# Kernel optimization log

Measured on AMD Instinct MI355X. Metric: run time of the kernel, lower is better.

The kernel has to match this reference:

```python
import jax, jax.numpy as jnp
import numpy as np

B, NA, DIN, H, DOUT = 8192, 32, 8, 64, 8  # B must be divisible by NA (final reshape)


def setup_inputs() -> dict:
    key = jax.random.key(0)
    ks = jax.random.split(key, 9)
    rn = lambda k, shp, s=1.0: jax.random.normal(k, shp, dtype=jnp.float32) * s
    return {
        "x": rn(ks[0], (B, NA, DIN)),
        "laplacian": jax.random.uniform(ks[1], (B, NA, 1), dtype=jnp.float32),
        "W_in": rn(ks[2], (H, DIN), 1.0 / np.sqrt(DIN)),
        "b_in": rn(ks[3], (H,), 0.01),
        "Aq": rn(ks[4], (H, H)),   # torch.randn init in original
        "Ak": rn(ks[5], (H, H)),
        "Av": rn(ks[6], (H, H)),
        "W_out": rn(ks[7], (DOUT, H), 1.0 / np.sqrt(H)),
        "b_out": rn(ks[8], (DOUT,), 0.01),
    }


def reference(x, laplacian, W_in, b_in, Aq, Ak, Av, W_out, b_out):
    silu = jax.nn.silu
    # mlp_in = SiLU(Linear); kron(laplacian, ones(1,1,H)) == broadcast of (B,na,1) mask
    h = silu(x @ W_in.T + b_in) * laplacian            # (B, na, H)
    # Q/K/V: weight @ h^T with swish; attention is over the HIDDEN axis (H x H scores)
    Q = silu(jnp.einsum('ij,bnj->bin', Aq, h))         # (B, H, na)
    K = silu(jnp.einsum('ij,bnj->bni', Ak, h))         # (B, na, H)
    V = silu(jnp.einsum('ij,bnj->bin', Av, h))         # (B, H, na)
    A = jax.nn.softmax(jnp.einsum('bin,bnj->bij', Q, K), axis=2)  # (B, H, H), softmax dim=2
    attn = silu(jnp.einsum('bij,bjn->bni', A, V))      # (B, na, H)
    # mlp_out = SiLU(Linear), masked again, mean over nodes, reshape (B/na, na, O)
    y = silu(attn @ W_out.T + b_out) * laplacian       # (B, na, O)
    return y.mean(axis=1).reshape(-1, NA, DOUT)        # (B/NA, NA, O)
```

## Files before the change

kernel.cpp:

```cpp
#include <hip/hip_runtime.h>

#define NB   8192
#define NA   32
#define DIN  8
#define HID  64
#define DOUT 8

typedef float     v4f __attribute__((ext_vector_type(4)));
typedef _Float16  v4h __attribute__((ext_vector_type(4)));

__device__ __forceinline__ float silu_f(float x) {
    return __fdividef(x, 1.0f + __expf(-x));
}

__device__ __forceinline__ v4h cvt4(v4f a) {
    v4h r;
    r[0] = (_Float16)a[0]; r[1] = (_Float16)a[1];
    r[2] = (_Float16)a[2]; r[3] = (_Float16)a[3];
    return r;
}

__device__ __forceinline__ v4h silu_cvt4(v4f a) {
    v4f s;
    s[0] = silu_f(a[0]); s[1] = silu_f(a[1]);
    s[2] = silu_f(a[2]); s[3] = silu_f(a[3]);
    return cvt4(s);
}

#define MFMA16(A, B, C) __builtin_amdgcn_mfma_f32_16x16x16f16((A), (B), (C), 0, 0, 0)

__global__ __launch_bounds__(512, 4) void attn_mfma_kernel(
    const float* __restrict__ x,
    const float* __restrict__ lap,
    const float* __restrict__ W_in,
    const float* __restrict__ b_in,
    const float* __restrict__ Aq,
    const float* __restrict__ Ak,
    const float* __restrict__ Av,
    const float* __restrict__ W_out,
    const float* __restrict__ b_out,
    float* __restrict__ out)
{
    __shared__ _Float16 wlds[3][16][64][4];
    __shared__ _Float16 hlds[8][4][64][4];

    const int t  = threadIdx.x;
    const int l  = t & 63;
    const int w  = t >> 6;
    const int lm = l & 15;
    const int lg = l >> 4;

    {
        const float* mats[3] = {Aq, Ak, Av};
        #pragma unroll
        for (int m = 0; m < 3; ++m) {
            #pragma unroll
            for (int f = 0; f < 2; ++f) {
                const int fid = w * 2 + f;
                const int it = fid >> 2, ks = fid & 3;
                v4f v = *(const v4f*)(mats[m] + (lm + 16 * it) * 64 + 16 * ks + 4 * lg);
                *(v4h*)&wlds[m][fid][l][0] = cvt4(v);
            }
        }
    }

    v4h zh = {};
    v4f zf = {};
    v4h winf[4];
    #pragma unroll
    for (int jt = 0; jt < 4; ++jt)
        winf[jt] = (lg < 2) ? cvt4(*(const v4f*)(W_in + (lm + 16 * jt) * 8 + 4 * lg)) : zh;
    v4h woutf[4];
    #pragma unroll
    for (int ks = 0; ks < 4; ++ks)
        woutf[ks] = (lm < 8) ? cvt4(*(const v4f*)(W_out + lm * 64 + 16 * ks + 4 * lg)) : zh;
    float binf[4];
    #pragma unroll
    for (int jt = 0; jt < 4; ++jt) binf[jt] = b_in[lm + 16 * jt];
    const float boutf = (lm < 8) ? b_out[lm] : 0.0f;

    __syncthreads();

    const int b = blockIdx.x * 8 + w;

    v4f lapv[2];
    lapv[0] = *(const v4f*)(lap + b * 32 + 4 * lg);
    lapv[1] = *(const v4f*)(lap + b * 32 + 16 + 4 * lg);

    v4h xf[2];
    #pragma unroll
    for (int nt = 0; nt < 2; ++nt)
        xf[nt] = (lg < 2) ? cvt4(*(const v4f*)(x + b * 256 + (lm + 16 * nt) * 8 + 4 * lg)) : zh;

    const int pr = l ^ lg;
    v4h hf[2][4];
    #pragma unroll
    for (int nt = 0; nt < 2; ++nt) {
        #pragma unroll
        for (int jt = 0; jt < 4; ++jt) {
            v4f hc = MFMA16(xf[nt], winf[jt], zf);
            #pragma unroll
            for (int r = 0; r < 4; ++r) {
                float hv = silu_f(hc[r] + binf[jt]) * lapv[nt][r];
                const int lr   = (4 * lg + r) | ((lm >> 2) << 4);
                const int phys = lr ^ (lm >> 2);
                hlds[w][jt][phys][lm & 3] = (_Float16)hv;
            }
        }
        __builtin_amdgcn_s_waitcnt(0);
        #pragma unroll
        for (int ks = 0; ks < 4; ++ks)
            hf[nt][ks] = *(v4h*)&hlds[w][ks][pr][0];
        __builtin_amdgcn_s_waitcnt(0);
    }

    v4h qf[2][4];
    {
        v4f acc[2][4] = {};
        #pragma unroll
        for (int it = 0; it < 4; ++it)
            #pragma unroll
            for (int ks = 0; ks < 4; ++ks) {
                v4h bw = *(v4h*)&wlds[0][it * 4 + ks][l][0];
                #pragma unroll
                for (int nt = 0; nt < 2; ++nt)
                    acc[nt][it] = MFMA16(hf[nt][ks], bw, acc[nt][it]);
            }
        #pragma unroll
        for (int nt = 0; nt < 2; ++nt)
            #pragma unroll
            for (int it = 0; it < 4; ++it) qf[nt][it] = silu_cvt4(acc[nt][it]);
    }
    v4h kf[2][4];
    {
        v4f acc[2][4] = {};
        #pragma unroll
        for (int it = 0; it < 4; ++it)
            #pragma unroll
            for (int ks = 0; ks < 4; ++ks) {
                v4h bw = *(v4h*)&wlds[1][it * 4 + ks][l][0];
                #pragma unroll
                for (int nt = 0; nt < 2; ++nt)
                    acc[nt][it] = MFMA16(hf[nt][ks], bw, acc[nt][it]);
            }
        #pragma unroll
        for (int nt = 0; nt < 2; ++nt)
            #pragma unroll
            for (int it = 0; it < 4; ++it) kf[nt][it] = silu_cvt4(acc[nt][it]);
    }
    v4h vf[4][2];
    {
        v4f acc[4][2] = {};
        #pragma unroll
        for (int it = 0; it < 4; ++it)
            #pragma unroll
            for (int ks = 0; ks < 4; ++ks) {
                v4h aw = *(v4h*)&wlds[2][it * 4 + ks][l][0];
                #pragma unroll
                for (int nt = 0; nt < 2; ++nt)
                    acc[it][nt] = MFMA16(aw, hf[nt][ks], acc[it][nt]);
            }
        #pragma unroll
        for (int it = 0; it < 4; ++it)
            #pragma unroll
            for (int nt = 0; nt < 2; ++nt) vf[it][nt] = silu_cvt4(acc[it][nt]);
    }

    v4f ya[2] = {};
    #pragma unroll
    for (int it = 0; it < 4; ++it) {
        v4f s[4] = {};
        #pragma unroll
        for (int jt = 0; jt < 4; ++jt)
            #pragma unroll
            for (int ns = 0; ns < 2; ++ns)
                s[jt] = MFMA16(kf[ns][jt], qf[ns][it], s[jt]);

        float mx = s[0][0];
        #pragma unroll
        for (int jt = 0; jt < 4; ++jt)
            #pragma unroll
            for (int r = 0; r < 4; ++r) mx = fmaxf(mx, s[jt][r]);
        mx = fmaxf(mx, __shfl_xor(mx, 16, 64));
        mx = fmaxf(mx, __shfl_xor(mx, 32, 64));
        float sum = 0.0f;
        #pragma unroll
        for (int jt = 0; jt < 4; ++jt)
            #pragma unroll
            for (int r = 0; r < 4; ++r) {
                float e = __expf(s[jt][r] - mx);
                s[jt][r] = e;
                sum += e;
            }
        sum += __shfl_xor(sum, 16, 64);
        sum += __shfl_xor(sum, 32, 64);
        const float inv = __fdividef(1.0f, sum);
        v4h pf[4];
        #pragma unroll
        for (int jt = 0; jt < 4; ++jt) pf[jt] = cvt4(s[jt] * inv);

        v4f pv[2] = {};
        #pragma unroll
        for (int js = 0; js < 4; ++js)
            #pragma unroll
            for (int nt = 0; nt < 2; ++nt)
                pv[nt] = MFMA16(pf[js], vf[js][nt], pv[nt]);

        #pragma unroll
        for (int nt = 0; nt < 2; ++nt)
            ya[nt] = MFMA16(silu_cvt4(pv[nt]), woutf[it], ya[nt]);
    }

    float acc = 0.0f;
    #pragma unroll
    for (int nt = 0; nt < 2; ++nt)
        #pragma unroll
        for (int r = 0; r < 4; ++r)
            acc += silu_f(ya[nt][r] + boutf) * lapv[nt][r];
    acc += __shfl_xor(acc, 16, 64);
    acc += __shfl_xor(acc, 32, 64);
    if (l < 8) out[b * DOUT + l] = acc * (1.0f / NA);
}

extern "C" void kernel_launch(void* const* d_in, const int* in_sizes, int n_in,
                              void* d_out, int out_size, void* d_ws, size_t ws_size,
                              hipStream_t stream) {
    const float* x     = (const float*)d_in[0];
    const float* lap   = (const float*)d_in[1];
    const float* W_in  = (const float*)d_in[2];
    const float* b_in  = (const float*)d_in[3];
    const float* Aq    = (const float*)d_in[4];
    const float* Ak    = (const float*)d_in[5];
    const float* Av    = (const float*)d_in[6];
    const float* W_out = (const float*)d_in[7];
    const float* b_out = (const float*)d_in[8];
    attn_mfma_kernel<<<1024, 512, 0, stream>>>(x, lap, W_in, b_in, Aq, Ak, Av,
                                               W_out, b_out, (float*)d_out);
}
```

Baseline: 60.21 us.

## Switch QKV, score and PV matmuls to 16x16x32 f16 MFMA

Replaces the 16x16x16 f16 MFMA instructions with the gfx950 16x16x32 variant for the Q/K/V projections, the score computation and the P·V product. Operand fragments are concatenated into 8-wide half vectors, and the LDS weight layout is rearranged so each lane holds 8 halves per fragment. This halves the number of MFMA issues and LDS weight reads along the K dimension. The correctness of the K-index mapping depends on how the concatenated fragments line up with the 32-wide instruction's lane layout.

```diff
diff --git a/kernel.cpp b/kernel.cpp
--- a/kernel.cpp
+++ b/kernel.cpp
@@ -8,6 +8,7 @@
 
 typedef float     v4f __attribute__((ext_vector_type(4)));
 typedef _Float16  v4h __attribute__((ext_vector_type(4)));
+typedef _Float16  v8h __attribute__((ext_vector_type(8)));
 
 __device__ __forceinline__ float silu_f(float x) {
     return __fdividef(x, 1.0f + __expf(-x));
@@ -20,6 +21,15 @@
     return r;
 }
 
+__device__ __forceinline__ v8h cvt8(v4f a, v4f b) {
+    v8h r;
+    r[0] = (_Float16)a[0]; r[1] = (_Float16)a[1];
+    r[2] = (_Float16)a[2]; r[3] = (_Float16)a[3];
+    r[4] = (_Float16)b[0]; r[5] = (_Float16)b[1];
+    r[6] = (_Float16)b[2]; r[7] = (_Float16)b[3];
+    return r;
+}
+
 __device__ __forceinline__ v4h silu_cvt4(v4f a) {
     v4f s;
     s[0] = silu_f(a[0]); s[1] = silu_f(a[1]);
@@ -27,7 +37,12 @@
     return cvt4(s);
 }
 
+__device__ __forceinline__ v8h cat(v4h a, v4h b) {
+    return __builtin_shufflevector(a, b, 0, 1, 2, 3, 4, 5, 6, 7);
+}
+
 #define MFMA16(A, B, C) __builtin_amdgcn_mfma_f32_16x16x16f16((A), (B), (C), 0, 0, 0)
+#define MFMA32(A, B, C) __builtin_amdgcn_mfma_f32_16x16x32_f16((A), (B), (C), 0, 0, 0)
 
 __global__ __launch_bounds__(512, 4) void attn_mfma_kernel(
     const float* __restrict__ x,
@@ -41,7 +56,7 @@
     const float* __restrict__ b_out,
     float* __restrict__ out)
 {
-    __shared__ _Float16 wlds[3][16][64][4];
+    __shared__ _Float16 wlds[3][8][64][8];
     __shared__ _Float16 hlds[8][4][64][4];
 
     const int t  = threadIdx.x;
@@ -52,15 +67,13 @@
 
     {
         const float* mats[3] = {Aq, Ak, Av};
+        const int it = w >> 1, c = w & 1;
         #pragma unroll
         for (int m = 0; m < 3; ++m) {
-            #pragma unroll
-            for (int f = 0; f < 2; ++f) {
-                const int fid = w * 2 + f;
-                const int it = fid >> 2, ks = fid & 3;
-                v4f v = *(const v4f*)(mats[m] + (lm + 16 * it) * 64 + 16 * ks + 4 * lg);
-                *(v4h*)&wlds[m][fid][l][0] = cvt4(v);
-            }
+            const float* base = mats[m] + (lm + 16 * it) * 64 + 32 * c + 4 * lg;
+            v4f va = *(const v4f*)(base);
+            v4f vb = *(const v4f*)(base + 16);
+            *(v8h*)&wlds[m][w][l][0] = cvt8(va, vb);
         }
     }
 
@@ -113,68 +126,71 @@
             hf[nt][ks] = *(v4h*)&hlds[w][ks][pr][0];
         __builtin_amdgcn_s_waitcnt(0);
     }
-
-    v4h qf[2][4];
+    v8h hf8[2][2];
+    #pragma unroll
+    for (int nt = 0; nt < 2; ++nt)
+        #pragma unroll
+        for (int c = 0; c < 2; ++c)
+            hf8[nt][c] = cat(hf[nt][2 * c], hf[nt][2 * c + 1]);
+
+    v8h qf8[4];
     {
         v4f acc[2][4] = {};
         #pragma unroll
         for (int it = 0; it < 4; ++it)
             #pragma unroll
-            for (int ks = 0; ks < 4; ++ks) {
-                v4h bw = *(v4h*)&wlds[0][it * 4 + ks][l][0];
+            for (int c = 0; c < 2; ++c) {
+                v8h bw = *(v8h*)&wlds[0][it * 2 + c][l][0];
                 #pragma unroll
                 for (int nt = 0; nt < 2; ++nt)
-                    acc[nt][it] = MFMA16(hf[nt][ks], bw, acc[nt][it]);
-            }
-        #pragma unroll
-        for (int nt = 0; nt < 2; ++nt)
-            #pragma unroll
-            for (int it = 0; it < 4; ++it) qf[nt][it] = silu_cvt4(acc[nt][it]);
-    }
-    v4h kf[2][4];
+                    acc[nt][it] = MFMA32(hf8[nt][c], bw, acc[nt][it]);
+            }
+        #pragma unroll
+        for (int it = 0; it < 4; ++it)
+            qf8[it] = cat(silu_cvt4(acc[0][it]), silu_cvt4(acc[1][it]));
+    }
+    v8h kf8[4];
     {
         v4f acc[2][4] = {};
         #pragma unroll
         for (int it = 0; it < 4; ++it)
             #pragma unroll
-            for (int ks = 0; ks < 4; ++ks) {
-                v4h bw = *(v4h*)&wlds[1][it * 4 + ks][l][0];
+            for (int c = 0; c < 2; ++c) {
+                v8h bw = *(v8h*)&wlds[1][it * 2 + c][l][0];
                 #pragma unroll
                 for (int nt = 0; nt < 2; ++nt)
-                    acc[nt][it] = MFMA16(hf[nt][ks], bw, acc[nt][it]);
-            }
-        #pragma unroll
-        for (int nt = 0; nt < 2; ++nt)
-            #pragma unroll
-            for (int it = 0; it < 4; ++it) kf[nt][it] = silu_cvt4(acc[nt][it]);
-    }
-    v4h vf[4][2];
+                    acc[nt][it] = MFMA32(hf8[nt][c], bw, acc[nt][it]);
+            }
+        #pragma unroll
+        for (int it = 0; it < 4; ++it)
+            kf8[it] = cat(silu_cvt4(acc[0][it]), silu_cvt4(acc[1][it]));
+    }
+    v8h vf8[2][2];
     {
         v4f acc[4][2] = {};
         #pragma unroll
         for (int it = 0; it < 4; ++it)
             #pragma unroll
-            for (int ks = 0; ks < 4; ++ks) {
-                v4h aw = *(v4h*)&wlds[2][it * 4 + ks][l][0];
+            for (int c = 0; c < 2; ++c) {
+                v8h aw = *(v8h*)&wlds[2][it * 2 + c][l][0];
                 #pragma unroll
                 for (int nt = 0; nt < 2; ++nt)
-                    acc[it][nt] = MFMA16(aw, hf[nt][ks], acc[it][nt]);
-            }
-        #pragma unroll
-        for (int it = 0; it < 4; ++it)
-            #pragma unroll
-            for (int nt = 0; nt < 2; ++nt) vf[it][nt] = silu_cvt4(acc[it][nt]);
+                    acc[it][nt] = MFMA32(aw, hf8[nt][c], acc[it][nt]);
+            }
+        #pragma unroll
+        for (int c = 0; c < 2; ++c)
+            #pragma unroll
+            for (int nt = 0; nt < 2; ++nt)
+                vf8[c][nt] = cat(silu_cvt4(acc[2 * c][nt]), silu_cvt4(acc[2 * c + 1][nt]));
     }
 
     v4f ya[2] = {};
     #pragma unroll
     for (int it = 0; it < 4; ++it) {
-        v4f s[4] = {};
+        v4f s[4];
         #pragma unroll
         for (int jt = 0; jt < 4; ++jt)
-            #pragma unroll
-            for (int ns = 0; ns < 2; ++ns)
-                s[jt] = MFMA16(kf[ns][jt], qf[ns][it], s[jt]);
+            s[jt] = MFMA32(kf8[jt], qf8[it], zf);
 
         float mx = s[0][0];
         #pragma unroll
@@ -201,10 +217,12 @@
 
         v4f pv[2] = {};
         #pragma unroll
-        for (int js = 0; js < 4; ++js)
+        for (int c = 0; c < 2; ++c) {
+            v8h pf8 = cat(pf[2 * c], pf[2 * c + 1]);
             #pragma unroll
             for (int nt = 0; nt < 2; ++nt)
-                pv[nt] = MFMA16(pf[js], vf[js][nt], pv[nt]);
+                pv[nt] = MFMA32(pf8, vf8[c][nt], pv[nt]);
+        }
 
         #pragma unroll
         for (int nt = 0; nt < 2; ++nt)
```

New measurement: 58.69 us. 2.5% less time.
